# Performance work log

Hardware: AMD Instinct MI355X
Metric: run time of the kernel (lower is better)

Reference implementation:

```python
import jax, jax.numpy as jnp
import numpy as np


def setup_inputs() -> dict:
    key = jax.random.key(0)
    k1, k2 = jax.random.split(key)
    B, N, M = 16, 4096, 4096
    xyz1 = jax.random.normal(k1, (B, N, 3), dtype=jnp.float32)
    xyz2 = jax.random.normal(k2, (B, M, 3), dtype=jnp.float32)
    return {"xyz1": xyz1, "xyz2": xyz2}


def reference(xyz1, xyz2):
    sq1 = jnp.sum(xyz1 * xyz1, axis=-1)            # [B, N]
    sq2 = jnp.sum(xyz2 * xyz2, axis=-1)            # [B, M]
    inner = jnp.einsum('bnd,bmd->bnm', xyz1, xyz2)  # [B, N, M]
    d = sq1[:, :, None] + sq2[:, None, :] - 2.0 * inner
    dist1 = jnp.min(d, axis=2)  # nearest in xyz2 for each point of xyz1, [B, N]
    dist2 = jnp.min(d, axis=1)  # nearest in xyz1 for each point of xyz2, [B, M]
    return (jnp.mean(dist1), jnp.mean(dist2))
```

## Files before the change

kernel.cpp:

```cpp
#include <hip/hip_runtime.h>
#include <float.h>

#define BATCH  16
#define NPTS   4096
#define TOTALP (BATCH * NPTS)
#define NQ     (2 * TOTALP)

typedef _Float16 half8  __attribute__((ext_vector_type(8)));
typedef float    f32x16 __attribute__((ext_vector_type(16)));

#define ONE2 0x3C003C00u

__device__ __forceinline__ unsigned enc(float f)
{
    unsigned b = __float_as_uint(f);
    return (b & 0x80000000u) ? ~b : (b | 0x80000000u);
}
__device__ __forceinline__ float dec(unsigned k)
{
    return (k & 0x80000000u) ? __uint_as_float(k & 0x7FFFFFFFu)
                             : __uint_as_float(~k);
}

__device__ __forceinline__ unsigned pk(_Float16 lo, _Float16 hi)
{
    const unsigned a = (unsigned)__builtin_bit_cast(unsigned short, lo);
    const unsigned b = (unsigned)__builtin_bit_cast(unsigned short, hi);
    return a | (b << 16);
}

__device__ __forceinline__ float min16(const f32x16& d, float acc)
{
    const float m1 = fminf(fminf(d[0],  d[1]),  d[2]);
    const float m2 = fminf(fminf(d[3],  d[4]),  d[5]);
    const float m3 = fminf(fminf(d[6],  d[7]),  d[8]);
    const float m4 = fminf(fminf(d[9],  d[10]), d[11]);
    const float m5 = fminf(fminf(d[12], d[13]), d[14]);
    const float m6 = fminf(fminf(m1, m2), m3);
    const float m7 = fminf(fminf(m4, m5), d[15]);
    return fminf(fminf(m6, m7), acc);
}

__global__ __launch_bounds__(256) void prep_kernel(
    const float* __restrict__ xyz1, const float* __restrict__ xyz2,
    uint4* __restrict__ packQ, uint4* __restrict__ planes,
    unsigned* __restrict__ keys, float* __restrict__ out)
{
    const int i = blockIdx.x * 256 + threadIdx.x;
    if (i == 0) { out[0] = 0.0f; out[1] = 0.0f; }
    keys[i] = 0xFFFFFFFFu;

    const float* src = (i < TOTALP) ? xyz1 : xyz2;
    const int p = i & (TOTALP - 1);
    const float x = src[3 * p + 0];
    const float y = src[3 * p + 1];
    const float z = src[3 * p + 2];
    const float sq = x * x + y * y + z * z;
    const _Float16 sh = (_Float16)sq;
    const _Float16 sl = (_Float16)(sq - (float)sh);

    const _Float16 vxh = (_Float16)x, vyh = (_Float16)y, vzh = (_Float16)z;
    const _Float16 vxl = (_Float16)(x - (float)vxh);
    const _Float16 vyl = (_Float16)(y - (float)vyh);
    const _Float16 vzl = (_Float16)(z - (float)vzh);
    planes[i]      = make_uint4(pk(vxh, vyh), pk(vzh, vxh),
                                pk(vyh, vzh), pk(vxl, vyl));
    planes[NQ + i] = make_uint4(pk(vzl, vxl), pk(vyl, vzl),
                                ONE2,         pk(sh, sl));

    const float ux = -2.0f * x, uy = -2.0f * y, uz = -2.0f * z;
    const _Float16 uxh = (_Float16)ux, uyh = (_Float16)uy, uzh = (_Float16)uz;
    const _Float16 uxl = (_Float16)(ux - (float)uxh);
    const _Float16 uyl = (_Float16)(uy - (float)uyh);
    const _Float16 uzl = (_Float16)(uz - (float)uzh);
    packQ[i] = make_uint4(pk(uxh, uyh), pk(uzh, uxl), pk(uyl, uzl), pk(sh, sl));
}

__global__ __launch_bounds__(256, 4) void chamfer_stream(
    const uint4* __restrict__ packQ, const uint4* __restrict__ planes,
    unsigned* __restrict__ keys)
{
    const int blk = blockIdx.x;
    const int ch  = blk & 7;
    const int qc  = (blk >> 3) & 3;
    const int b   = (blk >> 5) & 15;
    const int dir = blk >> 9;

    const int lane = threadIdx.x & 63;
    const int wv   = threadIdx.x >> 6;
    const int n32  = lane & 31;
    const int half = lane >> 5;

    const int qbase = dir * TOTALP + b * NPTS + qc * 1024 + wv * 256;
    half8 bfrag[8];
#pragma unroll
    for (int qf = 0; qf < 8; ++qf) {
        const uint4 d = packQ[qbase + qf * 32 + n32];
        const uint4 u = half ? make_uint4(d.y, d.z, d.w, ONE2)
                             : make_uint4(d.x, d.y, d.z, d.x);
        bfrag[qf] = __builtin_bit_cast(half8, u);
    }

    float acc[8];
#pragma unroll
    for (int qf = 0; qf < 8; ++qf) acc[qf] = FLT_MAX;

    f32x16 cz;
#pragma unroll
    for (int r = 0; r < 16; ++r) cz[r] = 0.0f;

    const uint4* __restrict__ ap =
        planes + (size_t)half * NQ + (dir ^ 1) * TOTALP + b * NPTS + ch * 512;

    uint4 t0 = ap[0 * 32 + n32];
    uint4 t1 = ap[1 * 32 + n32];
    uint4 t2 = ap[2 * 32 + n32];
    uint4 t3 = ap[3 * 32 + n32];

    for (int t = 0; t < 16; ++t) {
        const uint4 tn = ap[(((t + 4) & 15) * 32) + n32];
        const half8 af = __builtin_bit_cast(half8, t0);
#pragma unroll
        for (int qf = 0; qf < 8; ++qf) {
            const f32x16 dd = __builtin_amdgcn_mfma_f32_32x32x16_f16(
                af, bfrag[qf], cz, 0, 0, 0);
            acc[qf] = min16(dd, acc[qf]);
        }
        t0 = t1; t1 = t2; t2 = t3; t3 = tn;
    }

#pragma unroll
    for (int qf = 0; qf < 8; ++qf) {
        float v = acc[qf];
        v = fminf(v, __shfl_xor(v, 32));
        if (lane < 32)
            atomicMin(&keys[qbase + qf * 32 + n32], enc(v));
    }
}

__global__ __launch_bounds__(256) void chamfer_final_atomic(
    const unsigned* __restrict__ keys, float* __restrict__ out)
{
    const int q0  = blockIdx.x * 512 + threadIdx.x;
    const int dir = q0 >> 16;

    float d = dec(keys[q0]) + dec(keys[q0 + 256]);

    for (int off = 32; off > 0; off >>= 1)
        d += __shfl_down(d, off);

    __shared__ float wsum[4];
    const int lane = threadIdx.x & 63;
    const int wv   = threadIdx.x >> 6;
    if (lane == 0) wsum[wv] = d;
    __syncthreads();
    if (threadIdx.x == 0) {
        float s = wsum[0] + wsum[1] + wsum[2] + wsum[3];
        atomicAdd(&out[dir], s * (1.0f / (float)TOTALP));
    }
}

__global__ void zero_out_kernel(float* __restrict__ out)
{
    if (threadIdx.x == 0) { out[0] = 0.0f; out[1] = 0.0f; }
}

__global__ __launch_bounds__(256) void chamfer_raw_kernel(
    const float* __restrict__ xyz1, const float* __restrict__ xyz2,
    float* __restrict__ out)
{
    const int blk = blockIdx.x;
    const int dir = blk >> 8;
    const int idx = blk & 255;
    const int b   = idx >> 4;
    const int n0  = (idx & 15) << 8;

    const float* __restrict__ own = (dir == 0 ? xyz1 : xyz2) + (size_t)b * NPTS * 3;
    const float* __restrict__ opp = (dir == 0 ? xyz2 : xyz1) + (size_t)b * NPTS * 3;

    const int n = n0 + threadIdx.x;
    const float ax = own[3 * n + 0];
    const float ay = own[3 * n + 1];
    const float az = own[3 * n + 2];

    float best = FLT_MAX;
    for (int m = 0; m < NPTS; m += 4) {
#pragma unroll
        for (int u = 0; u < 4; ++u) {
            const float px = opp[3 * (m + u) + 0];
            const float py = opp[3 * (m + u) + 1];
            const float pz = opp[3 * (m + u) + 2];
            const float dx = px - ax, dy = py - ay, dz = pz - az;
            float d = dx * dx;
            d = fmaf(dy, dy, d);
            d = fmaf(dz, dz, d);
            best = fminf(best, d);
        }
    }

    float d = best;
    for (int off = 32; off > 0; off >>= 1)
        d += __shfl_down(d, off);

    __shared__ float wsum[4];
    const int lane = threadIdx.x & 63;
    const int wv   = threadIdx.x >> 6;
    if (lane == 0) wsum[wv] = d;
    __syncthreads();
    if (threadIdx.x == 0) {
        float s = wsum[0] + wsum[1] + wsum[2] + wsum[3];
        atomicAdd(&out[dir], s * (1.0f / (float)TOTALP));
    }
}

extern "C" void kernel_launch(void* const* d_in, const int* in_sizes, int n_in,
                              void* d_out, int out_size, void* d_ws, size_t ws_size,
                              hipStream_t stream)
{
    const float* xyz1 = (const float*)d_in[0];
    const float* xyz2 = (const float*)d_in[1];
    float* out = (float*)d_out;

    const size_t keys_bytes  = (size_t)NQ * sizeof(unsigned);
    const size_t packQ_bytes = (size_t)NQ * sizeof(uint4);
    const size_t plane_bytes = (size_t)2 * NQ * sizeof(uint4);

    if (ws_size >= keys_bytes + packQ_bytes + plane_bytes) {
        unsigned* keys   = (unsigned*)d_ws;
        uint4*    packQ  = (uint4*)((char*)d_ws + keys_bytes);
        uint4*    planes = (uint4*)((char*)d_ws + keys_bytes + packQ_bytes);

        prep_kernel<<<NQ / 256, 256, 0, stream>>>(xyz1, xyz2, packQ, planes, keys, out);
        chamfer_stream<<<1024, 256, 0, stream>>>(packQ, planes, keys);
        chamfer_final_atomic<<<NQ / 512, 256, 0, stream>>>(keys, out);
    } else {
        zero_out_kernel<<<1, 64, 0, stream>>>(out);
        chamfer_raw_kernel<<<512, 256, 0, stream>>>(xyz1, xyz2, out);
    }
}
```

Baseline: 83.33 us.

## Fuse prep, stream, and final reduction into one cooperative kernel with grid syncs

Merges the three kernel launches into a single cooperative kernel that uses grid.sync() between the prep, MFMA min-distance, and final reduction phases. The goal is to remove two kernel launch gaps. In exchange it adds two grid-wide barriers and needs all 1024 blocks to be co-resident. If the cooperative launch fails, it falls back to the original three-kernel path.

```diff
diff --git a/kernel.cpp b/kernel.cpp
--- a/kernel.cpp
+++ b/kernel.cpp
@@ -1,5 +1,8 @@
 #include <hip/hip_runtime.h>
+#include <hip/hip_cooperative_groups.h>
 #include <float.h>
+
+namespace cg = cooperative_groups;
 
 #define BATCH  16
 #define NPTS   4096
@@ -41,12 +44,12 @@
     return fminf(fminf(m6, m7), acc);
 }
 
-__global__ __launch_bounds__(256) void prep_kernel(
-    const float* __restrict__ xyz1, const float* __restrict__ xyz2,
+
+__device__ __forceinline__ void prep_body(
+    int i, const float* __restrict__ xyz1, const float* __restrict__ xyz2,
     uint4* __restrict__ packQ, uint4* __restrict__ planes,
     unsigned* __restrict__ keys, float* __restrict__ out)
 {
-    const int i = blockIdx.x * 256 + threadIdx.x;
     if (i == 0) { out[0] = 0.0f; out[1] = 0.0f; }
     keys[i] = 0xFFFFFFFFu;
 
@@ -76,11 +79,10 @@
     packQ[i] = make_uint4(pk(uxh, uyh), pk(uzh, uxl), pk(uyl, uzl), pk(sh, sl));
 }
 
-__global__ __launch_bounds__(256, 4) void chamfer_stream(
-    const uint4* __restrict__ packQ, const uint4* __restrict__ planes,
+__device__ __forceinline__ void stream_body(
+    int blk, const uint4* __restrict__ packQ, const uint4* __restrict__ planes,
     unsigned* __restrict__ keys)
 {
-    const int blk = blockIdx.x;
     const int ch  = blk & 7;
     const int qc  = (blk >> 3) & 3;
     const int b   = (blk >> 5) & 15;
@@ -136,6 +138,60 @@
         if (lane < 32)
             atomicMin(&keys[qbase + qf * 32 + n32], enc(v));
     }
+}
+
+__global__ __launch_bounds__(256, 4) void chamfer_coop(
+    const float* __restrict__ xyz1, const float* __restrict__ xyz2,
+    uint4* __restrict__ packQ, uint4* __restrict__ planes,
+    unsigned* __restrict__ keys, float* __restrict__ out)
+{
+    cg::grid_group grid = cg::this_grid();
+    __shared__ float wsum[4];
+
+    const int gtid = blockIdx.x * 256 + threadIdx.x;
+    if (gtid < NQ)
+        prep_body(gtid, xyz1, xyz2, packQ, planes, keys, out);
+
+    grid.sync();
+
+    stream_body(blockIdx.x, packQ, planes, keys);
+
+    grid.sync();
+
+    if (blockIdx.x < NQ / 512) {
+        const int q0  = blockIdx.x * 512 + threadIdx.x;
+        const int dir = q0 >> 16;
+
+        float d = dec(keys[q0]) + dec(keys[q0 + 256]);
+
+        for (int off = 32; off > 0; off >>= 1)
+            d += __shfl_down(d, off);
+
+        const int lane = threadIdx.x & 63;
+        const int wv   = threadIdx.x >> 6;
+        if (lane == 0) wsum[wv] = d;
+        __syncthreads();
+        if (threadIdx.x == 0) {
+            const float s = wsum[0] + wsum[1] + wsum[2] + wsum[3];
+            atomicAdd(&out[dir], s * (1.0f / (float)TOTALP));
+        }
+    }
+}
+
+__global__ __launch_bounds__(256) void prep_kernel(
+    const float* __restrict__ xyz1, const float* __restrict__ xyz2,
+    uint4* __restrict__ packQ, uint4* __restrict__ planes,
+    unsigned* __restrict__ keys, float* __restrict__ out)
+{
+    const int i = blockIdx.x * 256 + threadIdx.x;
+    prep_body(i, xyz1, xyz2, packQ, planes, keys, out);
+}
+
+__global__ __launch_bounds__(256, 4) void chamfer_stream(
+    const uint4* __restrict__ packQ, const uint4* __restrict__ planes,
+    unsigned* __restrict__ keys)
+{
+    stream_body(blockIdx.x, packQ, planes, keys);
 }
 
 __global__ __launch_bounds__(256) void chamfer_final_atomic(
@@ -230,9 +286,18 @@
         uint4*    packQ  = (uint4*)((char*)d_ws + keys_bytes);
         uint4*    planes = (uint4*)((char*)d_ws + keys_bytes + packQ_bytes);
 
-        prep_kernel<<<NQ / 256, 256, 0, stream>>>(xyz1, xyz2, packQ, planes, keys, out);
-        chamfer_stream<<<1024, 256, 0, stream>>>(packQ, planes, keys);
-        chamfer_final_atomic<<<NQ / 512, 256, 0, stream>>>(keys, out);
+        void* kargs[] = { (void*)&xyz1, (void*)&xyz2, (void*)&packQ,
+                          (void*)&planes, (void*)&keys, (void*)&out };
+        hipError_t e = hipLaunchCooperativeKernel(
+            (const void*)chamfer_coop, dim3(1024), dim3(256), kargs, 0, stream);
+
+        if (e != hipSuccess) {
+            (void)hipGetLastError();
+            prep_kernel<<<NQ / 256, 256, 0, stream>>>(
+                xyz1, xyz2, packQ, planes, keys, out);
+            chamfer_stream<<<1024, 256, 0, stream>>>(packQ, planes, keys);
+            chamfer_final_atomic<<<NQ / 512, 256, 0, stream>>>(keys, out);
+        }
     } else {
         zero_out_kernel<<<1, 64, 0, stream>>>(out);
         chamfer_raw_kernel<<<512, 256, 0, stream>>>(xyz1, xyz2, out);
```

Result: slower. 276.6 us (+231.9%).

## Fuse fp16 split packing into the MFMA chamfer kernel and drop prep buffers

Applied to the files above, without the earlier changes.

Removes the separate prep kernel that wrote packed fp16 hi/lo planes and query records to workspace. The stream kernel now reads raw float xyz directly and builds the A and B fragments in registers, and a small init kernel only resets keys and the output. This cuts one launch and the workspace write/read traffic. In exchange every block redoes the conversion of the opposing points inside the MFMA loop, and the loads become strided 12-byte float triples instead of 16-byte vectors.

```diff
diff --git a/kernel.cpp b/kernel.cpp
--- a/kernel.cpp
+++ b/kernel.cpp
@@ -41,43 +41,35 @@
     return fminf(fminf(m6, m7), acc);
 }
 
-__global__ __launch_bounds__(256) void prep_kernel(
-    const float* __restrict__ xyz1, const float* __restrict__ xyz2,
-    uint4* __restrict__ packQ, uint4* __restrict__ planes,
-    unsigned* __restrict__ keys, float* __restrict__ out)
-{
-    const int i = blockIdx.x * 256 + threadIdx.x;
-    if (i == 0) { out[0] = 0.0f; out[1] = 0.0f; }
-    keys[i] = 0xFFFFFFFFu;
-
-    const float* src = (i < TOTALP) ? xyz1 : xyz2;
-    const int p = i & (TOTALP - 1);
-    const float x = src[3 * p + 0];
-    const float y = src[3 * p + 1];
-    const float z = src[3 * p + 2];
+__device__ __forceinline__ uint4 arec(float x, float y, float z, int half)
+{
     const float sq = x * x + y * y + z * z;
     const _Float16 sh = (_Float16)sq;
     const _Float16 sl = (_Float16)(sq - (float)sh);
-
     const _Float16 vxh = (_Float16)x, vyh = (_Float16)y, vzh = (_Float16)z;
     const _Float16 vxl = (_Float16)(x - (float)vxh);
     const _Float16 vyl = (_Float16)(y - (float)vyh);
     const _Float16 vzl = (_Float16)(z - (float)vzh);
-    planes[i]      = make_uint4(pk(vxh, vyh), pk(vzh, vxh),
-                                pk(vyh, vzh), pk(vxl, vyl));
-    planes[NQ + i] = make_uint4(pk(vzl, vxl), pk(vyl, vzl),
-                                ONE2,         pk(sh, sl));
-
-    const float ux = -2.0f * x, uy = -2.0f * y, uz = -2.0f * z;
-    const _Float16 uxh = (_Float16)ux, uyh = (_Float16)uy, uzh = (_Float16)uz;
-    const _Float16 uxl = (_Float16)(ux - (float)uxh);
-    const _Float16 uyl = (_Float16)(uy - (float)uyh);
-    const _Float16 uzl = (_Float16)(uz - (float)uzh);
-    packQ[i] = make_uint4(pk(uxh, uyh), pk(uzh, uxl), pk(uyl, uzl), pk(sh, sl));
-}
-
-__global__ __launch_bounds__(256, 4) void chamfer_stream(
-    const uint4* __restrict__ packQ, const uint4* __restrict__ planes,
+    return half ? make_uint4(pk(vzl, vxl), pk(vyl, vzl), ONE2, pk(sh, sl))
+                : make_uint4(pk(vxh, vyh), pk(vzh, vxh), pk(vyh, vzh),
+                             pk(vxl, vyl));
+}
+
+__device__ __forceinline__ float3 ld3(const float* __restrict__ p, int idx)
+{
+    return make_float3(p[3 * idx + 0], p[3 * idx + 1], p[3 * idx + 2]);
+}
+
+__global__ __launch_bounds__(256) void init_kernel(
+    uint4* __restrict__ keys4, float* __restrict__ out)
+{
+    const int i = blockIdx.x * 256 + threadIdx.x;
+    keys4[i] = make_uint4(~0u, ~0u, ~0u, ~0u);
+    if (i == 0) { out[0] = 0.0f; out[1] = 0.0f; }
+}
+
+__global__ __launch_bounds__(256, 4) void chamfer_stream_fused(
+    const float* __restrict__ xyz1, const float* __restrict__ xyz2,
     unsigned* __restrict__ keys)
 {
     const int blk = blockIdx.x;
@@ -91,13 +83,31 @@
     const int n32  = lane & 31;
     const int half = lane >> 5;
 
-    const int qbase = dir * TOTALP + b * NPTS + qc * 1024 + wv * 256;
+    const float* __restrict__ qsrc = dir ? xyz2 : xyz1;
+    const float* __restrict__ osrc = dir ? xyz1 : xyz2;
+
+    const int qloc  = b * NPTS + qc * 1024 + wv * 256;
+    const int qbase = dir * TOTALP + qloc;
     half8 bfrag[8];
 #pragma unroll
     for (int qf = 0; qf < 8; ++qf) {
-        const uint4 d = packQ[qbase + qf * 32 + n32];
-        const uint4 u = half ? make_uint4(d.y, d.z, d.w, ONE2)
-                             : make_uint4(d.x, d.y, d.z, d.x);
+        const int qi = qloc + qf * 32 + n32;
+        const float x = qsrc[3 * qi + 0];
+        const float y = qsrc[3 * qi + 1];
+        const float z = qsrc[3 * qi + 2];
+        const float sq = x * x + y * y + z * z;
+        const _Float16 sh = (_Float16)sq;
+        const _Float16 sl = (_Float16)(sq - (float)sh);
+        const float ux = -2.0f * x, uy = -2.0f * y, uz = -2.0f * z;
+        const _Float16 uxh = (_Float16)ux, uyh = (_Float16)uy,
+                       uzh = (_Float16)uz;
+        const _Float16 uxl = (_Float16)(ux - (float)uxh);
+        const _Float16 uyl = (_Float16)(uy - (float)uyh);
+        const _Float16 uzl = (_Float16)(uz - (float)uzh);
+        const uint4 u = half
+            ? make_uint4(pk(uzh, uxl), pk(uyl, uzl), pk(sh, sl), ONE2)
+            : make_uint4(pk(uxh, uyh), pk(uzh, uxl), pk(uyl, uzl),
+                         pk(uxh, uyh));
         bfrag[qf] = __builtin_bit_cast(half8, u);
     }
 
@@ -109,17 +119,17 @@
 #pragma unroll
     for (int r = 0; r < 16; ++r) cz[r] = 0.0f;
 
-    const uint4* __restrict__ ap =
-        planes + (size_t)half * NQ + (dir ^ 1) * TOTALP + b * NPTS + ch * 512;
-
-    uint4 t0 = ap[0 * 32 + n32];
-    uint4 t1 = ap[1 * 32 + n32];
-    uint4 t2 = ap[2 * 32 + n32];
-    uint4 t3 = ap[3 * 32 + n32];
+    const float* __restrict__ op = osrc + (size_t)(b * NPTS + ch * 512) * 3;
+
+    float3 t0 = ld3(op, 0 * 32 + n32);
+    float3 t1 = ld3(op, 1 * 32 + n32);
+    float3 t2 = ld3(op, 2 * 32 + n32);
+    float3 t3 = ld3(op, 3 * 32 + n32);
 
     for (int t = 0; t < 16; ++t) {
-        const uint4 tn = ap[(((t + 4) & 15) * 32) + n32];
-        const half8 af = __builtin_bit_cast(half8, t0);
+        const float3 tn = ld3(op, ((t + 4) & 15) * 32 + n32);
+        const uint4 ar = arec(t0.x, t0.y, t0.z, half);
+        const half8 af = __builtin_bit_cast(half8, ar);
 #pragma unroll
         for (int qf = 0; qf < 8; ++qf) {
             const f32x16 dd = __builtin_amdgcn_mfma_f32_32x32x16_f16(
@@ -221,17 +231,13 @@
     const float* xyz2 = (const float*)d_in[1];
     float* out = (float*)d_out;
 
-    const size_t keys_bytes  = (size_t)NQ * sizeof(unsigned);
-    const size_t packQ_bytes = (size_t)NQ * sizeof(uint4);
-    const size_t plane_bytes = (size_t)2 * NQ * sizeof(uint4);
-
-    if (ws_size >= keys_bytes + packQ_bytes + plane_bytes) {
-        unsigned* keys   = (unsigned*)d_ws;
-        uint4*    packQ  = (uint4*)((char*)d_ws + keys_bytes);
-        uint4*    planes = (uint4*)((char*)d_ws + keys_bytes + packQ_bytes);
-
-        prep_kernel<<<NQ / 256, 256, 0, stream>>>(xyz1, xyz2, packQ, planes, keys, out);
-        chamfer_stream<<<1024, 256, 0, stream>>>(packQ, planes, keys);
+    const size_t keys_bytes = (size_t)NQ * sizeof(unsigned);
+
+    if (ws_size >= keys_bytes) {
+        unsigned* keys = (unsigned*)d_ws;
+
+        init_kernel<<<NQ / 4 / 256, 256, 0, stream>>>((uint4*)keys, out);
+        chamfer_stream_fused<<<1024, 256, 0, stream>>>(xyz1, xyz2, keys);
         chamfer_final_atomic<<<NQ / 512, 256, 0, stream>>>(keys, out);
     } else {
         zero_out_kernel<<<1, 64, 0, stream>>>(out);
```

Result: no change. 82.99 us (-0.4%).
